# Kernel optimization log

Hardware: AMD Instinct MI355X
Metric: run time of the kernel (lower is better)

Reference implementation:

```python
import jax, jax.numpy as jnp
import numpy as np

B, T, D = 8, 128, 256


def setup_inputs() -> dict:
    key = jax.random.key(0)
    k1, k2 = jax.random.split(key)
    dec_t = jax.random.normal(k1, (B, D), dtype=jnp.float32)
    enc_out = jax.random.normal(k2, (B, T, D), dtype=jnp.float32)
    return {"dec_t": dec_t, "enc_out": enc_out}


def reference(dec_t, enc_out):
    # Faithful vectorization of the original double Python loop.
    # Per timestep t: E[b,p,q] = exp(dec_t[b,p] * enc_out[b,t,q])  (outer product)
    # a_ts[b,p,q] = E[b,p,q] / rowsum[b,q]   (torch broadcast [D,D]/[D] divides
    #               each column q by the row-sum of row q: rowsum[q]=sum_r E[q,r])
    # contribution to c_t: a_ts[b,p,q] * enc_out[b,t,q], accumulated over t,
    # then summed over p.
    # => c_t[b,q] = sum_t enc_out[b,t,q] * colsum[b,t,q] / rowsum[b,t,q]
    E = jnp.exp(dec_t[:, None, :, None] * enc_out[:, :, None, :])  # [B,T,D,D]
    colsum = E.sum(axis=2)  # sum over p -> [B,T,D] indexed by q
    rowsum = E.sum(axis=3)  # sum over r -> [B,T,D] indexed by q (row q of outer)
    return jnp.sum(enc_out * colsum / rowsum, axis=1)  # [B,D]
```

## Files before the change

### kernel.cpp

```cpp
#include <hip/hip_runtime.h>

#define BB 8
#define TT 128
#define DD 256
#define LOG2E 1.44269504088896340736f

__global__ __launch_bounds__(256, 4) void attn_sym_kernel(
    const float* __restrict__ dec,
    const float* __restrict__ enc,
    float* __restrict__ ws) {
    const int blk = blockIdx.x;
    const int b = blk >> 7;
    const int tid = threadIdx.x;

    const float* __restrict__ drow = dec + b * DD;
    const float* __restrict__ erow = enc + blk * DD;

    const float dv = drow[tid];
    const float ev = erow[tid];
    const float dl2 = dv * LOG2E;
    const float el2 = ev * LOG2E;

    float cs0 = 0.f, cs1 = 0.f, cs2 = 0.f, cs3 = 0.f;
    float rs0 = 0.f, rs1 = 0.f, rs2 = 0.f, rs3 = 0.f;
    #pragma unroll 8
    for (int k = 0; k < DD; k += 4) {
        float4 d4 = *reinterpret_cast<const float4*>(drow + k);
        float4 e4 = *reinterpret_cast<const float4*>(erow + k);
        cs0 += __builtin_amdgcn_exp2f(d4.x * el2);
        cs1 += __builtin_amdgcn_exp2f(d4.y * el2);
        cs2 += __builtin_amdgcn_exp2f(d4.z * el2);
        cs3 += __builtin_amdgcn_exp2f(d4.w * el2);
        rs0 += __builtin_amdgcn_exp2f(dl2 * e4.x);
        rs1 += __builtin_amdgcn_exp2f(dl2 * e4.y);
        rs2 += __builtin_amdgcn_exp2f(dl2 * e4.z);
        rs3 += __builtin_amdgcn_exp2f(dl2 * e4.w);
    }
    const float cs = (cs0 + cs1) + (cs2 + cs3);
    const float rs = (rs0 + rs1) + (rs2 + rs3);

    ws[blk * DD + tid] = ev * cs / rs;
}

__global__ __launch_bounds__(256) void reduce_t_kernel(
    const float* __restrict__ ws, float* __restrict__ out) {
    __shared__ float red[4][64];
    const int b = blockIdx.x >> 2;
    const int qc = blockIdx.x & 3;
    const int qlane = threadIdx.x & 63;
    const int tc = threadIdx.x >> 6;
    const int q = qc * 64 + qlane;

    const float* p = ws + (b * TT + tc * 32) * DD + q;
    float a0 = 0.f, a1 = 0.f, a2 = 0.f, a3 = 0.f;
    #pragma unroll
    for (int t = 0; t < 32; t += 4) {
        a0 += p[(t + 0) * DD];
        a1 += p[(t + 1) * DD];
        a2 += p[(t + 2) * DD];
        a3 += p[(t + 3) * DD];
    }
    red[tc][qlane] = (a0 + a1) + (a2 + a3);
    __syncthreads();
    if (tc == 0)
        out[b * DD + q] = red[0][qlane] + red[1][qlane] +
                          red[2][qlane] + red[3][qlane];
}

extern "C" void kernel_launch(void* const* d_in, const int* in_sizes, int n_in,
                              void* d_out, int out_size, void* d_ws, size_t ws_size,
                              hipStream_t stream) {
    const float* dec = (const float*)d_in[0];
    const float* enc = (const float*)d_in[1];
    float* out = (float*)d_out;
    float* ws = (float*)d_ws;

    attn_sym_kernel<<<BB * TT, 256, 0, stream>>>(dec, enc, ws);
    reduce_t_kernel<<<BB * 4, 256, 0, stream>>>(ws, out);
}
```

Measured before the change: 70.73 us.

## Share each exp between row and column sums via 16x16 outer-product tiles

Each thread now computes a 16x16 tile of the exponentiated outer product, and each exp value feeds both the column-sum and the row-sum accumulation. Before, every element was exponentiated twice. Partial sums are staged in shared memory and reduced after a barrier. This halves transcendental work per block but adds LDS traffic, a sync and more register pressure.

Measured after the change: 88.22 us. +24.7%, slower.

```diff
diff --git a/kernel.cpp b/kernel.cpp
--- a/kernel.cpp
+++ b/kernel.cpp
@@ -5,41 +5,85 @@
 #define DD 256
 #define LOG2E 1.44269504088896340736f
 
-__global__ __launch_bounds__(256, 4) void attn_sym_kernel(
+__global__ __launch_bounds__(256, 4) void attn_tile16_kernel(
     const float* __restrict__ dec,
     const float* __restrict__ enc,
     float* __restrict__ ws) {
+    __shared__ float srow[DD * 17];
+    __shared__ float scol[16 * 260];
+
     const int blk = blockIdx.x;
     const int b = blk >> 7;
     const int tid = threadIdx.x;
+    const int tx = tid & 15;
+    const int ty = tid >> 4;
 
-    const float* __restrict__ drow = dec + b * DD;
-    const float* __restrict__ erow = enc + blk * DD;
+    const float* __restrict__ drow = dec + b * DD + ty * 16;
+    const float* __restrict__ erow = enc + blk * DD + tx * 16;
 
-    const float dv = drow[tid];
-    const float ev = erow[tid];
-    const float dl2 = dv * LOG2E;
-    const float el2 = ev * LOG2E;
+    const float4 dv0 = *reinterpret_cast<const float4*>(drow + 0);
+    const float4 dv1 = *reinterpret_cast<const float4*>(drow + 4);
+    const float4 dv2 = *reinterpret_cast<const float4*>(drow + 8);
+    const float4 dv3 = *reinterpret_cast<const float4*>(drow + 12);
+    const float4 ev0 = *reinterpret_cast<const float4*>(erow + 0);
+    const float4 ev1 = *reinterpret_cast<const float4*>(erow + 4);
+    const float4 ev2 = *reinterpret_cast<const float4*>(erow + 8);
+    const float4 ev3 = *reinterpret_cast<const float4*>(erow + 12);
 
-    float cs0 = 0.f, cs1 = 0.f, cs2 = 0.f, cs3 = 0.f;
-    float rs0 = 0.f, rs1 = 0.f, rs2 = 0.f, rs3 = 0.f;
-    #pragma unroll 8
-    for (int k = 0; k < DD; k += 4) {
-        float4 d4 = *reinterpret_cast<const float4*>(drow + k);
-        float4 e4 = *reinterpret_cast<const float4*>(erow + k);
-        cs0 += __builtin_amdgcn_exp2f(d4.x * el2);
-        cs1 += __builtin_amdgcn_exp2f(d4.y * el2);
-        cs2 += __builtin_amdgcn_exp2f(d4.z * el2);
-        cs3 += __builtin_amdgcn_exp2f(d4.w * el2);
-        rs0 += __builtin_amdgcn_exp2f(dl2 * e4.x);
-        rs1 += __builtin_amdgcn_exp2f(dl2 * e4.y);
-        rs2 += __builtin_amdgcn_exp2f(dl2 * e4.z);
-        rs3 += __builtin_amdgcn_exp2f(dl2 * e4.w);
-    }
-    const float cs = (cs0 + cs1) + (cs2 + cs3);
-    const float rs = (rs0 + rs1) + (rs2 + rs3);
+    const float d0 = dv0.x * LOG2E, d1 = dv0.y * LOG2E, d2 = dv0.z * LOG2E, d3 = dv0.w * LOG2E;
+    const float d4 = dv1.x * LOG2E, d5 = dv1.y * LOG2E, d6 = dv1.z * LOG2E, d7 = dv1.w * LOG2E;
+    const float d8 = dv2.x * LOG2E, d9 = dv2.y * LOG2E, d10 = dv2.z * LOG2E, d11 = dv2.w * LOG2E;
+    const float d12 = dv3.x * LOG2E, d13 = dv3.y * LOG2E, d14 = dv3.z * LOG2E, d15 = dv3.w * LOG2E;
+    const float e0 = ev0.x, e1 = ev0.y, e2 = ev0.z, e3 = ev0.w;
+    const float e4 = ev1.x, e5 = ev1.y, e6 = ev1.z, e7 = ev1.w;
+    const float e8 = ev2.x, e9 = ev2.y, e10 = ev2.z, e11 = ev2.w;
+    const float e12 = ev3.x, e13 = ev3.y, e14 = ev3.z, e15 = ev3.w;
 
-    ws[blk * DD + tid] = ev * cs / rs;
+    float c0 = 0.f, c1 = 0.f, c2 = 0.f, c3 = 0.f, c4 = 0.f, c5 = 0.f, c6 = 0.f, c7 = 0.f;
+    float c8 = 0.f, c9 = 0.f, c10 = 0.f, c11 = 0.f, c12 = 0.f, c13 = 0.f, c14 = 0.f, c15 = 0.f;
+
+#define ROW(I, DI) { \
+    float ra, rb, x; \
+    x = __builtin_amdgcn_exp2f(DI * e0);  c0  += x; ra  = x; \
+    x = __builtin_amdgcn_exp2f(DI * e1);  c1  += x; ra += x; \
+    x = __builtin_amdgcn_exp2f(DI * e2);  c2  += x; ra += x; \
+    x = __builtin_amdgcn_exp2f(DI * e3);  c3  += x; ra += x; \
+    x = __builtin_amdgcn_exp2f(DI * e4);  c4  += x; ra += x; \
+    x = __builtin_amdgcn_exp2f(DI * e5);  c5  += x; ra += x; \
+    x = __builtin_amdgcn_exp2f(DI * e6);  c6  += x; ra += x; \
+    x = __builtin_amdgcn_exp2f(DI * e7);  c7  += x; ra += x; \
+    x = __builtin_amdgcn_exp2f(DI * e8);  c8  += x; rb  = x; \
+    x = __builtin_amdgcn_exp2f(DI * e9);  c9  += x; rb += x; \
+    x = __builtin_amdgcn_exp2f(DI * e10); c10 += x; rb += x; \
+    x = __builtin_amdgcn_exp2f(DI * e11); c11 += x; rb += x; \
+    x = __builtin_amdgcn_exp2f(DI * e12); c12 += x; rb += x; \
+    x = __builtin_amdgcn_exp2f(DI * e13); c13 += x; rb += x; \
+    x = __builtin_amdgcn_exp2f(DI * e14); c14 += x; rb += x; \
+    x = __builtin_amdgcn_exp2f(DI * e15); c15 += x; rb += x; \
+    srow[(ty * 16 + (I)) * 17 + tx] = ra + rb; \
+}
+    ROW(0, d0)   ROW(1, d1)   ROW(2, d2)   ROW(3, d3)
+    ROW(4, d4)   ROW(5, d5)   ROW(6, d6)   ROW(7, d7)
+    ROW(8, d8)   ROW(9, d9)   ROW(10, d10) ROW(11, d11)
+    ROW(12, d12) ROW(13, d13) ROW(14, d14) ROW(15, d15)
+#undef ROW
+
+    *reinterpret_cast<float4*>(&scol[ty * 260 + tx * 16 + 0])  = make_float4(c0, c1, c2, c3);
+    *reinterpret_cast<float4*>(&scol[ty * 260 + tx * 16 + 4])  = make_float4(c4, c5, c6, c7);
+    *reinterpret_cast<float4*>(&scol[ty * 260 + tx * 16 + 8])  = make_float4(c8, c9, c10, c11);
+    *reinterpret_cast<float4*>(&scol[ty * 260 + tx * 16 + 12]) = make_float4(c12, c13, c14, c15);
+    __syncthreads();
+
+    const float* sr = srow + tid * 17;
+    float rs = ((sr[0] + sr[1]) + (sr[2] + sr[3])) + ((sr[4] + sr[5]) + (sr[6] + sr[7]))
+             + ((sr[8] + sr[9]) + (sr[10] + sr[11])) + ((sr[12] + sr[13]) + (sr[14] + sr[15]));
+    float cs = ((scol[0*260+tid] + scol[1*260+tid]) + (scol[2*260+tid] + scol[3*260+tid]))
+             + ((scol[4*260+tid] + scol[5*260+tid]) + (scol[6*260+tid] + scol[7*260+tid]))
+             + ((scol[8*260+tid] + scol[9*260+tid]) + (scol[10*260+tid] + scol[11*260+tid]))
+             + ((scol[12*260+tid] + scol[13*260+tid]) + (scol[14*260+tid] + scol[15*260+tid]));
+
+    const float eq = enc[blk * DD + tid];
+    ws[blk * DD + tid] = eq * cs / rs;
 }
 
 __global__ __launch_bounds__(256) void reduce_t_kernel(
@@ -75,6 +119,6 @@
     float* out = (float*)d_out;
     float* ws = (float*)d_ws;
 
-    attn_sym_kernel<<<BB * TT, 256, 0, stream>>>(dec, enc, ws);
+    attn_tile16_kernel<<<BB * TT, 256, 0, stream>>>(dec, enc, ws);
     reduce_t_kernel<<<BB * 4, 256, 0, stream>>>(ws, out);
 }
```

## Fuse T-reduction into compute kernel via per-block time chunks and atomics

Applied to the files above, without the earlier changes.

Each block now handles four timesteps for one batch, accumulates them in registers, and atomically adds the result into the output after a small zeroing kernel. This removes the workspace round-trip and the separate reduction kernel. The grid shrinks from 1024 to 256 blocks, which lowers parallelism for an exp-bound kernel, and the fp32 atomics make summation order nondeterministic.

New measurement: 76.01 us. 1.07x slower.

```diff
diff --git a/kernel.cpp b/kernel.cpp
--- a/kernel.cpp
+++ b/kernel.cpp
@@ -3,68 +3,54 @@
 #define BB 8
 #define TT 128
 #define DD 256
+#define TC 4
 #define LOG2E 1.44269504088896340736f
 
-__global__ __launch_bounds__(256, 4) void attn_sym_kernel(
+__global__ __launch_bounds__(256) void zero_out_kernel(float* __restrict__ out) {
+    int i = blockIdx.x * blockDim.x + threadIdx.x;
+    if (i < BB * DD) out[i] = 0.0f;
+}
+
+__global__ __launch_bounds__(256) void attn_atomic_kernel(
     const float* __restrict__ dec,
     const float* __restrict__ enc,
-    float* __restrict__ ws) {
-    const int blk = blockIdx.x;
-    const int b = blk >> 7;
+    float* __restrict__ out) {
+    const int b  = blockIdx.x >> 5;
+    const int tc = blockIdx.x & 31;
     const int tid = threadIdx.x;
 
     const float* __restrict__ drow = dec + b * DD;
-    const float* __restrict__ erow = enc + blk * DD;
+    const float dl2 = drow[tid] * LOG2E;
 
-    const float dv = drow[tid];
-    const float ev = erow[tid];
-    const float dl2 = dv * LOG2E;
-    const float el2 = ev * LOG2E;
+    float acc = 0.0f;
+    #pragma unroll
+    for (int tt = 0; tt < TC; ++tt) {
+        const int t = tc * TC + tt;
+        const float* __restrict__ erow = enc + (b * TT + t) * DD;
+        const float ev = erow[tid];
+        const float el2 = ev * LOG2E;
 
-    float cs0 = 0.f, cs1 = 0.f, cs2 = 0.f, cs3 = 0.f;
-    float rs0 = 0.f, rs1 = 0.f, rs2 = 0.f, rs3 = 0.f;
-    #pragma unroll 8
-    for (int k = 0; k < DD; k += 4) {
-        float4 d4 = *reinterpret_cast<const float4*>(drow + k);
-        float4 e4 = *reinterpret_cast<const float4*>(erow + k);
-        cs0 += __builtin_amdgcn_exp2f(d4.x * el2);
-        cs1 += __builtin_amdgcn_exp2f(d4.y * el2);
-        cs2 += __builtin_amdgcn_exp2f(d4.z * el2);
-        cs3 += __builtin_amdgcn_exp2f(d4.w * el2);
-        rs0 += __builtin_amdgcn_exp2f(dl2 * e4.x);
-        rs1 += __builtin_amdgcn_exp2f(dl2 * e4.y);
-        rs2 += __builtin_amdgcn_exp2f(dl2 * e4.z);
-        rs3 += __builtin_amdgcn_exp2f(dl2 * e4.w);
+        float cs0 = 0.f, cs1 = 0.f, cs2 = 0.f, cs3 = 0.f;
+        float rs0 = 0.f, rs1 = 0.f, rs2 = 0.f, rs3 = 0.f;
+        #pragma unroll 8
+        for (int k = 0; k < DD; k += 4) {
+            float4 d4 = *reinterpret_cast<const float4*>(drow + k);
+            float4 e4 = *reinterpret_cast<const float4*>(erow + k);
+            cs0 += __builtin_amdgcn_exp2f(d4.x * el2);
+            cs1 += __builtin_amdgcn_exp2f(d4.y * el2);
+            cs2 += __builtin_amdgcn_exp2f(d4.z * el2);
+            cs3 += __builtin_amdgcn_exp2f(d4.w * el2);
+            rs0 += __builtin_amdgcn_exp2f(dl2 * e4.x);
+            rs1 += __builtin_amdgcn_exp2f(dl2 * e4.y);
+            rs2 += __builtin_amdgcn_exp2f(dl2 * e4.z);
+            rs3 += __builtin_amdgcn_exp2f(dl2 * e4.w);
+        }
+        const float cs = (cs0 + cs1) + (cs2 + cs3);
+        const float rs = (rs0 + rs1) + (rs2 + rs3);
+        acc += ev * cs / rs;
     }
-    const float cs = (cs0 + cs1) + (cs2 + cs3);
-    const float rs = (rs0 + rs1) + (rs2 + rs3);
 
-    ws[blk * DD + tid] = ev * cs / rs;
-}
-
-__global__ __launch_bounds__(256) void reduce_t_kernel(
-    const float* __restrict__ ws, float* __restrict__ out) {
-    __shared__ float red[4][64];
-    const int b = blockIdx.x >> 2;
-    const int qc = blockIdx.x & 3;
-    const int qlane = threadIdx.x & 63;
-    const int tc = threadIdx.x >> 6;
-    const int q = qc * 64 + qlane;
-
-    const float* p = ws + (b * TT + tc * 32) * DD + q;
-    float a0 = 0.f, a1 = 0.f, a2 = 0.f, a3 = 0.f;
-    #pragma unroll
-    for (int t = 0; t < 32; t += 4) {
-        a0 += p[(t + 0) * DD];
-        a1 += p[(t + 1) * DD];
-        a2 += p[(t + 2) * DD];
-        a3 += p[(t + 3) * DD];
-    }
-    red[tc][qlane] = (a0 + a1) + (a2 + a3);
-    __syncthreads();
-    if (tc == 0)
-        out[b * DD + q] = red[0][qlane] + red[1][qlane] +
-                          red[2][qlane] + red[3][qlane];
+    atomicAdd(&out[b * DD + tid], acc);
 }
 
 extern "C" void kernel_launch(void* const* d_in, const int* in_sizes, int n_in,
@@ -73,8 +59,8 @@
     const float* dec = (const float*)d_in[0];
     const float* enc = (const float*)d_in[1];
     float* out = (float*)d_out;
-    float* ws = (float*)d_ws;
+    (void)d_ws; (void)ws_size;
 
-    attn_sym_kernel<<<BB * TT, 256, 0, stream>>>(dec, enc, ws);
-    reduce_t_kernel<<<BB * 4, 256, 0, stream>>>(ws, out);
+    zero_out_kernel<<<BB, 256, 0, stream>>>(out);
+    attn_atomic_kernel<<<BB * (TT / TC), 256, 0, stream>>>(dec, enc, out);
 }
```
